# Performance work log

Hardware: AMD Instinct MI355X
Metric: run time of the kernel (lower is better)

## Reference

```python
import jax, jax.numpy as jnp
import numpy as np

N_VOCAB = 100      # periodic-table embedding size
N_GAUSS = 300      # SchNet-standard RBF expansion
RBF_CUTOFF = 30.0
RBF_GAMMA = 10.0
N_INTERACTIONS = 3
LOG2 = float(np.log(2.0))


def ssp(x):
    # shifted softplus: log(0.5*exp(x) + 0.5) = softplus(x) - log(2)
    return jax.nn.softplus(x) - LOG2


def setup_inputs() -> dict:
    key = jax.random.key(0)
    ks = jax.random.split(key, 16)
    B, N, F, NF = 32, 128, 128, 128
    s = lambda k, shape, sc=0.1: (jax.random.normal(k, shape, dtype=jnp.float32) * sc)
    return {
        "z": jax.random.randint(ks[0], (B, N), 0, N_VOCAB),
        "r": jax.random.normal(ks[1], (B, N, 3), dtype=jnp.float32) * 3.0,
        "emb": s(ks[2], (N_VOCAB, F)),
        "w_in2f": s(ks[3], (F, NF)),
        "w_f1": s(ks[4], (N_GAUSS, NF)), "b_f1": jnp.zeros((NF,), jnp.float32),
        "w_f2": s(ks[5], (NF, NF)),      "b_f2": jnp.zeros((NF,), jnp.float32),
        "w_f2out": s(ks[6], (NF, F)),    "b_f2out": jnp.zeros((F,), jnp.float32),
        "w_out": s(ks[7], (F, F)),       "b_out": jnp.zeros((F,), jnp.float32),
        "w_aw1": s(ks[8], (F, F)),       "b_aw1": jnp.zeros((F,), jnp.float32),
        "w_aw2": s(ks[9], (F, 1)),       "b_aw2": jnp.zeros((1,), jnp.float32),
    }


def reference(z, r, emb, w_in2f, w_f1, b_f1, w_f2, b_f2,
              w_f2out, b_f2out, w_out, b_out, w_aw1, b_aw1, w_aw2, b_aw2):
    # ---- pairwise distances + RBF expansion (shared across interactions) ----
    diff = r[:, :, None, :] - r[:, None, :, :]            # [B,N,N,3]
    d = jnp.sqrt(jnp.sum(diff * diff, axis=-1) + 1e-12)    # [B,N,N]
    centers = jnp.linspace(0.0, RBF_CUTOFF, N_GAUSS, dtype=jnp.float32)
    rbf = jnp.exp(-RBF_GAMMA * (d[..., None] - centers) ** 2)  # [B,N,N,G]
    # filter network (distance-only -> hoisted out of the interaction loop;
    # the single InteractionLayer is weight-shared across all passes)
    W = ssp(jnp.einsum('bijg,gf->bijf', rbf, w_f1) + b_f1)
    W = jnp.einsum('bijf,fh->bijh', W, w_f2) + b_f2         # [B,N,N,NF]

    # ---- atom embedding ----
    x = emb[z]                                              # [B,N,F]

    # ---- interaction blocks (shared weights, applied n_interactions times) ----
    for _ in range(N_INTERACTIONS):
        f = jnp.einsum('bnf,fh->bnh', x, w_in2f)            # atom-wise, no bias
        y = jnp.einsum('bijh,bjh->bih', W, f)               # cfconv aggregation
        y = ssp(jnp.einsum('bnh,hf->bnf', y, w_f2out) + b_f2out)
        v = jnp.einsum('bnf,fg->bng', y, w_out) + b_out
        x = x + v                                           # residual update

    # ---- atom-wise readout ----
    x = ssp(jnp.einsum('bnf,fg->bng', x, w_aw1) + b_aw1)
    out = jnp.einsum('bnf,fo->bno', x, w_aw2) + b_aw2       # [B,N,1]
    return out
```

## Files before the change

kernel.cpp:

```cpp
#include <hip/hip_runtime.h>
#include <hip/hip_bf16.h>
#include <stdint.h>

typedef __bf16 bf16x8 __attribute__((ext_vector_type(8)));
typedef float  f32x4  __attribute__((ext_vector_type(4)));
typedef unsigned short u16;
typedef unsigned int   u32;
typedef u16 u16x4 __attribute__((ext_vector_type(4)));
typedef u32 u32x4 __attribute__((ext_vector_type(4)));

#define B_  32
#define N_  128
#define F_  128
#define G_  300
#define GP  320
#define TAB_N 4096
#define TAB_SCALE 128.0f

__device__ __forceinline__ u16 f2b(float f){
  union { float f; u32 u; } x; x.f = f;
  u32 r = x.u + 0x7FFFu + ((x.u >> 16) & 1u);
  return (u16)(r >> 16);
}
__device__ __forceinline__ u32 pack2bf(float a, float b){
  return __builtin_amdgcn_perm(__float_as_uint(b) + 0x8000u,
                               __float_as_uint(a) + 0x8000u, 0x07060302u);
}
__device__ __forceinline__ float sspf(float x){
  return fmaxf(x, 0.0f) + __logf(0.5f + 0.5f*__expf(-fabsf(x)));
}
__device__ __forceinline__ f32x4 mfma16(bf16x8 a, bf16x8 b, f32x4 c){
  return __builtin_amdgcn_mfma_f32_16x16x32_bf16(a, b, c, 0, 0, 0);
}

__global__ __launch_bounds__(256) void k_setup(const float* __restrict__ w_f1,
                                               const float* __restrict__ w_f2,
                                               const float* __restrict__ w_in2f,
                                               const float* __restrict__ w_f2out,
                                               const float* __restrict__ w_out,
                                               const float* __restrict__ w_aw1,
                                               u16* __restrict__ w1t,
                                               u16* __restrict__ w2t,
                                               u16* __restrict__ wi2t,
                                               u16* __restrict__ w2outT,
                                               u16* __restrict__ woutT,
                                               u16* __restrict__ waw1T){
  int idx = blockIdx.x*256 + threadIdx.x;
  if (idx < 128*GP){
    int h = idx / GP, g = idx % GP;
    w1t[idx] = (g < G_) ? f2b(w_f1[g*F_ + h]) : (u16)0;
  } else {
    int j = idx - 128*GP;
    int which = j >> 14;
    int rr = j & 16383;
    int h = rr >> 7, k = rr & 127;
    const float* src; u16* dst;
    switch (which){
      case 0:  src = w_f2;    dst = w2t;    break;
      case 1:  src = w_in2f;  dst = wi2t;   break;
      case 2:  src = w_f2out; dst = w2outT; break;
      case 3:  src = w_out;   dst = woutT;  break;
      default: src = w_aw1;   dst = waw1T;  break;
    }
    dst[h*128 + k] = f2b(src[k*128 + h]);
  }
}

__global__ __launch_bounds__(256) void k_prep(const u16* __restrict__ w1t,
                                              const u16* __restrict__ w2t,
                                              const float* __restrict__ b_f1,
                                              const float* __restrict__ b_f2,
                                              u16* __restrict__ tab,
                                              const int* __restrict__ z,
                                              const float* __restrict__ emb,
                                              const u16* __restrict__ wi2t,
                                              u16* __restrict__ fb,
                                              const float* __restrict__ r,
                                              u16* __restrict__ dIdx){
  __shared__ __attribute__((aligned(16))) u16 w1s[16][136];
  __shared__ float rshp[128][3];
  int blk = blockIdx.x;
  int tid = threadIdx.x, lane = tid & 63, wave = tid >> 6;
  int m = lane & 15, q = lane >> 4;

  if (blk < 256){
    int t0 = blk * 16;
    int C0 = wave*32;
    const float K2 = 14.4269504089f;
    const float DC = 30.0f/299.0f;
    float d = (float)(t0 + m) * (1.0f/TAB_SCALE);
    f32x4 acc[2];
    acc[0] = (f32x4){0.f,0.f,0.f,0.f}; acc[1] = (f32x4){0.f,0.f,0.f,0.f};
    #pragma unroll
    for (int ks = 0; ks < 10; ++ks){
      int kb = ks*32 + q*8;
      u32x4 au;
      #pragma unroll
      for (int t2 = 0; t2 < 4; ++t2){
        int k0 = kb + t2*2;
        float u0 = d - DC*(float)k0;
        float u1 = d - DC*(float)(k0 + 1);
        float e0 = __builtin_amdgcn_exp2f(-K2*u0*u0);
        float e1 = __builtin_amdgcn_exp2f(-K2*u1*u1);
        au[t2] = pack2bf(e0, e1);
      }
      bf16x8 af = __builtin_bit_cast(bf16x8, au);
      #pragma unroll
      for (int ni = 0; ni < 2; ++ni){
        bf16x8 bfv = *reinterpret_cast<const bf16x8*>(w1t + (size_t)(C0 + ni*16 + m)*GP + kb);
        acc[ni] = mfma16(af, bfv, acc[ni]);
      }
    }
    #pragma unroll
    for (int ni = 0; ni < 2; ++ni)
      #pragma unroll
      for (int rr = 0; rr < 4; ++rr){
        int col = C0 + ni*16 + m;
        w1s[q*4 + rr][col & 127] = f2b(sspf(acc[ni][rr] + b_f1[col]));
      }
    __syncthreads();
    f32x4 acc2[2];
    acc2[0] = (f32x4){0.f,0.f,0.f,0.f}; acc2[1] = (f32x4){0.f,0.f,0.f,0.f};
    #pragma unroll
    for (int ks = 0; ks < 4; ++ks){
      int kb = ks*32 + q*8;
      bf16x8 af = *reinterpret_cast<const bf16x8*>(&w1s[m][kb]);
      #pragma unroll
      for (int ni = 0; ni < 2; ++ni){
        bf16x8 bfv = *reinterpret_cast<const bf16x8*>(w2t + (size_t)(C0 + ni*16 + m)*128 + kb);
        acc2[ni] = mfma16(af, bfv, acc2[ni]);
      }
    }
    #pragma unroll
    for (int ni = 0; ni < 2; ++ni)
      #pragma unroll
      for (int rr = 0; rr < 4; ++rr){
        int col = C0 + ni*16 + m;
        tab[(size_t)(t0 + q*4 + rr)*F_ + col] = f2b(acc2[ni][rr] + b_f2[col]);
      }
  } else if (blk < 384){
    int bi = blk - 256;
    int b = bi >> 2, qd = bi & 3;
    int R0 = qd*32 + (wave >> 1)*16;
    int C0 = (wave & 1)*64;
    int row = R0 + m;
    const float* erow = emb + (size_t)z[b*N_ + row]*F_;
    f32x4 acc[4];
    #pragma unroll
    for (int ni = 0; ni < 4; ++ni) acc[ni] = (f32x4){0.f,0.f,0.f,0.f};
    #pragma unroll
    for (int ks = 0; ks < 4; ++ks){
      int k0 = ks*32 + q*8;
      float4 e0 = *reinterpret_cast<const float4*>(erow + k0);
      float4 e1 = *reinterpret_cast<const float4*>(erow + k0 + 4);
      u32x4 au;
      au[0] = pack2bf(e0.x, e0.y); au[1] = pack2bf(e0.z, e0.w);
      au[2] = pack2bf(e1.x, e1.y); au[3] = pack2bf(e1.z, e1.w);
      bf16x8 af = __builtin_bit_cast(bf16x8, au);
      #pragma unroll
      for (int ni = 0; ni < 4; ++ni){
        bf16x8 bfv = *reinterpret_cast<const bf16x8*>(wi2t + (size_t)(C0 + ni*16 + m)*F_ + k0);
        acc[ni] = mfma16(af, bfv, acc[ni]);
      }
    }
    u16* fbb = fb + (size_t)b*N_*F_;
    #pragma unroll
    for (int ni = 0; ni < 4; ++ni)
      #pragma unroll
      for (int rr = 0; rr < 4; ++rr)
        fbb[(size_t)(R0 + q*4 + rr)*F_ + C0 + ni*16 + m] = f2b(acc[ni][rr]);
  } else {
    int pb = blk - 384;
    int b = pb >> 1, i0p = (pb & 1)*64;
    if (tid < 128){
      const float* rp = r + (size_t)(b*N_ + tid)*3;
      rshp[tid][0] = rp[0]; rshp[tid][1] = rp[1]; rshp[tid][2] = rp[2];
    }
    __syncthreads();
    #pragma unroll
    for (int t = 0; t < 32; ++t){
      int p = t*256 + tid;
      int il = p >> 7, j = p & 127;
      int i = i0p + il;
      float dx = rshp[i][0] - rshp[j][0];
      float dy = rshp[i][1] - rshp[j][1];
      float dz = rshp[i][2] - rshp[j][2];
      float d = sqrtf(fmaf(dx,dx, fmaf(dy,dy, fmaf(dz,dz, 1e-12f))));
      int ix = (int)(d * TAB_SCALE + 0.5f);
      if (ix > TAB_N - 1) ix = TAB_N - 1;
      dIdx[((size_t)(b*N_ + i))*N_ + j] = (u16)ix;
    }
  }
}

__global__ __launch_bounds__(256, 8) void k_conv(const u16* __restrict__ fb,
                                                 const u16* __restrict__ tab,
                                                 const u16* __restrict__ dIdx,
                                                 u16* __restrict__ yb){
  __shared__ u16 dIdxS[2][128];
  __shared__ __attribute__((aligned(16))) float psh[8][2][128];
  int bid = blockIdx.x;
  int b = bid >> 6, i0 = (bid & 63)*2;
  int tid = threadIdx.x;
  {
    int il = tid >> 7, j = tid & 127;
    dIdxS[il][j] = dIdx[((size_t)(b*N_ + i0 + il))*N_ + j];
  }
  __syncthreads();

  int chg = tid & 15, il = (tid >> 4) & 1, jq = tid >> 5;
  int h0 = chg*8;
  const u16* tb0 = tab + h0;
  const u16* fbp = fb + (size_t)b*N_*F_ + h0;
  float yv[8] = {0,0,0,0,0,0,0,0};
  #pragma unroll 8
  for (int jj = 0; jj < 16; ++jj){
    int j = jq*16 + jj;
    u32 ix = dIdxS[il][j];
    bf16x8 ta = *reinterpret_cast<const bf16x8*>(tb0 + ((size_t)ix << 7));
    bf16x8 fv = *reinterpret_cast<const bf16x8*>(fbp + (size_t)j*F_);
    #pragma unroll
    for (int t = 0; t < 8; ++t)
      yv[t] = fmaf((float)ta[t], (float)fv[t], yv[t]);
  }
  {
    float* pp = &psh[jq][il][h0];
    *reinterpret_cast<float4*>(pp)     = (float4){yv[0], yv[1], yv[2], yv[3]};
    *reinterpret_cast<float4*>(pp + 4) = (float4){yv[4], yv[5], yv[6], yv[7]};
  }
  __syncthreads();
  int ilo = tid >> 7, cho = tid & 127;
  float s = 0.f;
  #pragma unroll
  for (int t = 0; t < 8; ++t) s += psh[t][ilo][cho];
  yb[((size_t)(b*N_ + i0 + ilo))*F_ + cho] = f2b(s);
}

__global__ __launch_bounds__(512) void k_mlp(const u16* __restrict__ yb,
                                             float* __restrict__ x,
                                             const int* __restrict__ z,
                                             const float* __restrict__ emb,
                                             const u16* __restrict__ w2outT,
                                             const float* __restrict__ b_f2out,
                                             const u16* __restrict__ woutT,
                                             const float* __restrict__ b_out,
                                             const u16* __restrict__ wi2t,
                                             const u16* __restrict__ waw1T,
                                             const float* __restrict__ b_aw1,
                                             const float* __restrict__ w_aw2,
                                             const float* __restrict__ b_aw2,
                                             u16* __restrict__ fb,
                                             float* __restrict__ outp,
                                             int first, int mode){
  __shared__ __attribute__((aligned(16))) u16 ab[16][136];
  __shared__ float cs[16][132];
  __shared__ float psum[16][8];
  __shared__ int zsh[16];
  int tid = threadIdx.x, lane = tid & 63, wave = tid >> 6;
  int m = lane & 15, q = lane >> 4;
  int bid = blockIdx.x;
  int b = bid >> 3, R0 = (bid & 7)*16;
  int C0 = wave*16;
  int col = C0 + m;

  if (first && tid < 16) zsh[tid] = z[b*N_ + R0 + tid];
  {
    int row = tid >> 5, c4 = (tid & 31)*4;
    *reinterpret_cast<u16x4*>(&ab[row][c4]) =
      *reinterpret_cast<const u16x4*>(yb + ((size_t)(b*N_ + R0 + row))*F_ + c4);
  }
  __syncthreads();

  f32x4 acc = (f32x4){0.f,0.f,0.f,0.f};
  #pragma unroll
  for (int ks = 0; ks < 4; ++ks){
    int kb = ks*32 + q*8;
    bf16x8 af = *reinterpret_cast<const bf16x8*>(&ab[m][kb]);
    bf16x8 bfv = *reinterpret_cast<const bf16x8*>(w2outT + (size_t)col*F_ + kb);
    acc = mfma16(af, bfv, acc);
  }
  __syncthreads();
  #pragma unroll
  for (int rr = 0; rr < 4; ++rr)
    ab[q*4 + rr][col] = f2b(sspf(acc[rr] + b_f2out[col]));
  __syncthreads();

  f32x4 acc2 = (f32x4){0.f,0.f,0.f,0.f};
  #pragma unroll
  for (int ks = 0; ks < 4; ++ks){
    int kb = ks*32 + q*8;
    bf16x8 af = *reinterpret_cast<const bf16x8*>(&ab[m][kb]);
    bf16x8 bfv = *reinterpret_cast<const bf16x8*>(woutT + (size_t)col*F_ + kb);
    acc2 = mfma16(af, bfv, acc2);
  }
  __syncthreads();
  #pragma unroll
  for (int rr = 0; rr < 4; ++rr){
    int row = q*4 + rr;
    size_t xo = (size_t)(b*N_ + R0 + row)*F_ + col;
    float xi = first ? emb[(size_t)zsh[row]*F_ + col] : x[xo];
    float nv = xi + acc2[rr] + b_out[col];
    if (mode == 0) x[xo] = nv;
    ab[row][col] = f2b(nv);
  }
  __syncthreads();

  const u16* w3 = (mode == 0) ? wi2t : waw1T;
  f32x4 acc3 = (f32x4){0.f,0.f,0.f,0.f};
  #pragma unroll
  for (int ks = 0; ks < 4; ++ks){
    int kb = ks*32 + q*8;
    bf16x8 af = *reinterpret_cast<const bf16x8*>(&ab[m][kb]);
    bf16x8 bfv = *reinterpret_cast<const bf16x8*>(w3 + (size_t)col*F_ + kb);
    acc3 = mfma16(af, bfv, acc3);
  }
  if (mode == 0){
    #pragma unroll
    for (int rr = 0; rr < 4; ++rr)
      fb[(size_t)(b*N_ + R0 + q*4 + rr)*F_ + col] = f2b(acc3[rr]);
  } else {
    #pragma unroll
    for (int rr = 0; rr < 4; ++rr)
      cs[q*4 + rr][col] = sspf(acc3[rr] + b_aw1[col]) * w_aw2[col];
    __syncthreads();
    if (tid < 128){
      int row = tid >> 3, seg = tid & 7;
      float s = 0.f;
      #pragma unroll
      for (int t = 0; t < 16; ++t) s += cs[row][seg*16 + t];
      psum[row][seg] = s;
    }
    __syncthreads();
    if (tid < 16){
      float s = 0.f;
      #pragma unroll
      for (int t = 0; t < 8; ++t) s += psum[tid][t];
      outp[b*N_ + R0 + tid] = s + b_aw2[0];
    }
  }
}

extern "C" void kernel_launch(void* const* d_in, const int* in_sizes, int n_in,
                              void* d_out, int out_size, void* d_ws, size_t ws_size,
                              hipStream_t stream){
  const int*   z       = (const int*)d_in[0];
  const float* r       = (const float*)d_in[1];
  const float* emb     = (const float*)d_in[2];
  const float* w_in2f  = (const float*)d_in[3];
  const float* w_f1    = (const float*)d_in[4];
  const float* b_f1    = (const float*)d_in[5];
  const float* w_f2    = (const float*)d_in[6];
  const float* b_f2    = (const float*)d_in[7];
  const float* w_f2out = (const float*)d_in[8];
  const float* b_f2out = (const float*)d_in[9];
  const float* w_out   = (const float*)d_in[10];
  const float* b_out   = (const float*)d_in[11];
  const float* w_aw1   = (const float*)d_in[12];
  const float* b_aw1   = (const float*)d_in[13];
  const float* w_aw2   = (const float*)d_in[14];
  const float* b_aw2   = (const float*)d_in[15];

  char* ws = (char*)d_ws;
  float* x     = (float*)(ws);
  u16*   yb    = (u16*)(ws + 2097152);
  u16*   fbuf  = (u16*)(ws + 3145728);
  u16*   tab   = (u16*)(ws + 4194304);
  u16*   dIdx  = (u16*)(ws + 5242880);
  u16*   w1t   = (u16*)(ws + 6291456);
  u16*   w2t   = (u16*)(ws + 6373376);
  u16*   wi2t  = (u16*)(ws + 6406144);
  u16*   w2oT  = (u16*)(ws + 6438912);
  u16*   woT   = (u16*)(ws + 6471680);
  u16*   waw1T = (u16*)(ws + 6504448);

  k_setup<<<480, 256, 0, stream>>>(w_f1, w_f2, w_in2f, w_f2out, w_out, w_aw1,
                                   w1t, w2t, wi2t, w2oT, woT, waw1T);
  k_prep<<<448, 256, 0, stream>>>(w1t, w2t, b_f1, b_f2, tab,
                                  z, emb, wi2t, fbuf, r, dIdx);
  k_conv<<<2048, 256, 0, stream>>>(fbuf, tab, dIdx, yb);
  k_mlp<<<256, 512, 0, stream>>>(yb, x, z, emb, w2oT, b_f2out, woT, b_out,
                                 wi2t, waw1T, b_aw1, w_aw2, b_aw2,
                                 fbuf, (float*)d_out, 1, 0);
  k_conv<<<2048, 256, 0, stream>>>(fbuf, tab, dIdx, yb);
  k_mlp<<<256, 512, 0, stream>>>(yb, x, z, emb, w2oT, b_f2out, woT, b_out,
                                 wi2t, waw1T, b_aw1, w_aw2, b_aw2,
                                 fbuf, (float*)d_out, 0, 0);
  k_conv<<<2048, 256, 0, stream>>>(fbuf, tab, dIdx, yb);
  k_mlp<<<256, 512, 0, stream>>>(yb, x, z, emb, w2oT, b_f2out, woT, b_out,
                                 wi2t, waw1T, b_aw1, w_aw2, b_aw2,
                                 fbuf, (float*)d_out, 0, 1);
}
```

Before: 146.8 us.

## Fuse cfconv aggregation and atom-wise MLP into one per-iteration kernel

```diff
diff --git a/kernel.cpp b/kernel.cpp
--- a/kernel.cpp
+++ b/kernel.cpp
@@ -21,6 +21,9 @@
   union { float f; u32 u; } x; x.f = f;
   u32 r = x.u + 0x7FFFu + ((x.u >> 16) & 1u);
   return (u16)(r >> 16);
+}
+__device__ __forceinline__ float b2f(u16 v){
+  union { u32 u; float f; } x; x.u = ((u32)v) << 16; return x.f;
 }
 __device__ __forceinline__ u32 pack2bf(float a, float b){
   return __builtin_amdgcn_perm(__float_as_uint(b) + 0x8000u,
@@ -42,27 +45,31 @@
                                                u16* __restrict__ w1t,
                                                u16* __restrict__ w2t,
                                                u16* __restrict__ wi2t,
-                                               u16* __restrict__ w2outT,
-                                               u16* __restrict__ woutT,
-                                               u16* __restrict__ waw1T){
+                                               u16* __restrict__ wf2o,
+                                               u16* __restrict__ wob,
+                                               u16* __restrict__ wi2fb,
+                                               u16* __restrict__ waw1b){
   int idx = blockIdx.x*256 + threadIdx.x;
   if (idx < 128*GP){
     int h = idx / GP, g = idx % GP;
     w1t[idx] = (g < G_) ? f2b(w_f1[g*F_ + h]) : (u16)0;
+  } else if (idx < 128*GP + 32768){
+    int j = idx - 128*GP;
+    int which = j >> 14, rr = j & 16383;
+    int h = rr >> 7, k = rr & 127;
+    if (which == 0) w2t[h*128 + k]  = f2b(w_f2[k*128 + h]);
+    else            wi2t[h*128 + k] = f2b(w_in2f[k*128 + h]);
   } else {
-    int j = idx - 128*GP;
-    int which = j >> 14;
-    int rr = j & 16383;
-    int h = rr >> 7, k = rr & 127;
+    int j = idx - 128*GP - 32768;
+    int which = j >> 14, rr = j & 16383;
     const float* src; u16* dst;
     switch (which){
-      case 0:  src = w_f2;    dst = w2t;    break;
-      case 1:  src = w_in2f;  dst = wi2t;   break;
-      case 2:  src = w_f2out; dst = w2outT; break;
-      case 3:  src = w_out;   dst = woutT;  break;
-      default: src = w_aw1;   dst = waw1T;  break;
-    }
-    dst[h*128 + k] = f2b(src[k*128 + h]);
+      case 0:  src = w_f2out; dst = wf2o;  break;
+      case 1:  src = w_out;   dst = wob;   break;
+      case 2:  src = w_in2f;  dst = wi2fb; break;
+      default: src = w_aw1;   dst = waw1b; break;
+    }
+    dst[rr] = f2b(src[rr]);
   }
 }
 
@@ -193,12 +200,22 @@
   }
 }
 
-__global__ __launch_bounds__(256, 8) void k_conv(const u16* __restrict__ fb,
-                                                 const u16* __restrict__ tab,
-                                                 const u16* __restrict__ dIdx,
-                                                 u16* __restrict__ yb){
+__global__ __launch_bounds__(256, 8) void k_iter(
+    const u16* __restrict__ fb_in, const u16* __restrict__ tab,
+    const u16* __restrict__ dIdx,
+    float* __restrict__ x, const int* __restrict__ z,
+    const float* __restrict__ emb,
+    const u16* __restrict__ wf2o, const float* __restrict__ b_f2out,
+    const u16* __restrict__ wob,  const float* __restrict__ b_out,
+    const u16* __restrict__ wi2fb, const u16* __restrict__ waw1b,
+    const float* __restrict__ b_aw1, const float* __restrict__ w_aw2,
+    const float* __restrict__ b_aw2,
+    u16* __restrict__ fb_out, float* __restrict__ outp, int first, int mode){
   __shared__ u16 dIdxS[2][128];
   __shared__ __attribute__((aligned(16))) float psh[8][2][128];
+  __shared__ float ysh[2][132];
+  __shared__ float y2sh[2][132];
+  __shared__ float xsh[2][132];
   int bid = blockIdx.x;
   int b = bid >> 6, i0 = (bid & 63)*2;
   int tid = threadIdx.x;
@@ -208,134 +225,114 @@
   }
   __syncthreads();
 
-  int chg = tid & 15, il = (tid >> 4) & 1, jq = tid >> 5;
-  int h0 = chg*8;
-  const u16* tb0 = tab + h0;
-  const u16* fbp = fb + (size_t)b*N_*F_ + h0;
-  float yv[8] = {0,0,0,0,0,0,0,0};
-  #pragma unroll 8
-  for (int jj = 0; jj < 16; ++jj){
-    int j = jq*16 + jj;
-    u32 ix = dIdxS[il][j];
-    bf16x8 ta = *reinterpret_cast<const bf16x8*>(tb0 + ((size_t)ix << 7));
-    bf16x8 fv = *reinterpret_cast<const bf16x8*>(fbp + (size_t)j*F_);
-    #pragma unroll
-    for (int t = 0; t < 8; ++t)
-      yv[t] = fmaf((float)ta[t], (float)fv[t], yv[t]);
-  }
-  {
+  {
+    int chg = tid & 15, il = (tid >> 4) & 1, jq = tid >> 5;
+    int h0 = chg*8;
+    const u16* tb0 = tab + h0;
+    const u16* fbp = fb_in + (size_t)b*N_*F_ + h0;
+    float yv[8] = {0,0,0,0,0,0,0,0};
+    #pragma unroll 8
+    for (int jj = 0; jj < 16; ++jj){
+      int j = jq*16 + jj;
+      u32 ix = dIdxS[il][j];
+      bf16x8 ta = *reinterpret_cast<const bf16x8*>(tb0 + ((size_t)ix << 7));
+      bf16x8 fv = *reinterpret_cast<const bf16x8*>(fbp + (size_t)j*F_);
+      #pragma unroll
+      for (int t = 0; t < 8; ++t)
+        yv[t] = fmaf((float)ta[t], (float)fv[t], yv[t]);
+    }
     float* pp = &psh[jq][il][h0];
     *reinterpret_cast<float4*>(pp)     = (float4){yv[0], yv[1], yv[2], yv[3]};
     *reinterpret_cast<float4*>(pp + 4) = (float4){yv[4], yv[5], yv[6], yv[7]};
   }
   __syncthreads();
-  int ilo = tid >> 7, cho = tid & 127;
-  float s = 0.f;
-  #pragma unroll
-  for (int t = 0; t < 8; ++t) s += psh[t][ilo][cho];
-  yb[((size_t)(b*N_ + i0 + ilo))*F_ + cho] = f2b(s);
-}
-
-__global__ __launch_bounds__(512) void k_mlp(const u16* __restrict__ yb,
-                                             float* __restrict__ x,
-                                             const int* __restrict__ z,
-                                             const float* __restrict__ emb,
-                                             const u16* __restrict__ w2outT,
-                                             const float* __restrict__ b_f2out,
-                                             const u16* __restrict__ woutT,
-                                             const float* __restrict__ b_out,
-                                             const u16* __restrict__ wi2t,
-                                             const u16* __restrict__ waw1T,
-                                             const float* __restrict__ b_aw1,
-                                             const float* __restrict__ w_aw2,
-                                             const float* __restrict__ b_aw2,
-                                             u16* __restrict__ fb,
-                                             float* __restrict__ outp,
-                                             int first, int mode){
-  __shared__ __attribute__((aligned(16))) u16 ab[16][136];
-  __shared__ float cs[16][132];
-  __shared__ float psum[16][8];
-  __shared__ int zsh[16];
-  int tid = threadIdx.x, lane = tid & 63, wave = tid >> 6;
-  int m = lane & 15, q = lane >> 4;
-  int bid = blockIdx.x;
-  int b = bid >> 3, R0 = (bid & 7)*16;
-  int C0 = wave*16;
-  int col = C0 + m;
-
-  if (first && tid < 16) zsh[tid] = z[b*N_ + R0 + tid];
-  {
-    int row = tid >> 5, c4 = (tid & 31)*4;
-    *reinterpret_cast<u16x4*>(&ab[row][c4]) =
-      *reinterpret_cast<const u16x4*>(yb + ((size_t)(b*N_ + R0 + row))*F_ + c4);
-  }
-  __syncthreads();
-
-  f32x4 acc = (f32x4){0.f,0.f,0.f,0.f};
-  #pragma unroll
-  for (int ks = 0; ks < 4; ++ks){
-    int kb = ks*32 + q*8;
-    bf16x8 af = *reinterpret_cast<const bf16x8*>(&ab[m][kb]);
-    bf16x8 bfv = *reinterpret_cast<const bf16x8*>(w2outT + (size_t)col*F_ + kb);
-    acc = mfma16(af, bfv, acc);
-  }
-  __syncthreads();
-  #pragma unroll
-  for (int rr = 0; rr < 4; ++rr)
-    ab[q*4 + rr][col] = f2b(sspf(acc[rr] + b_f2out[col]));
-  __syncthreads();
-
-  f32x4 acc2 = (f32x4){0.f,0.f,0.f,0.f};
-  #pragma unroll
-  for (int ks = 0; ks < 4; ++ks){
-    int kb = ks*32 + q*8;
-    bf16x8 af = *reinterpret_cast<const bf16x8*>(&ab[m][kb]);
-    bf16x8 bfv = *reinterpret_cast<const bf16x8*>(woutT + (size_t)col*F_ + kb);
-    acc2 = mfma16(af, bfv, acc2);
-  }
-  __syncthreads();
-  #pragma unroll
-  for (int rr = 0; rr < 4; ++rr){
-    int row = q*4 + rr;
-    size_t xo = (size_t)(b*N_ + R0 + row)*F_ + col;
-    float xi = first ? emb[(size_t)zsh[row]*F_ + col] : x[xo];
-    float nv = xi + acc2[rr] + b_out[col];
+  {
+    int ilo = tid >> 7, cho = tid & 127;
+    float s = 0.f;
+    #pragma unroll
+    for (int t = 0; t < 8; ++t) s += psh[t][ilo][cho];
+    ysh[ilo][cho] = s;
+  }
+  __syncthreads();
+
+  int kh = tid >> 7, col = tid & 127;
+  int k0 = kh*64;
+  float* psum = &psh[0][0][0];
+
+  {
+    float a0 = 0.f, a1 = 0.f;
+    #pragma unroll 8
+    for (int kk = 0; kk < 64; ++kk){
+      int k = k0 + kk;
+      float w = b2f(wf2o[k*F_ + col]);
+      a0 = fmaf(ysh[0][k], w, a0);
+      a1 = fmaf(ysh[1][k], w, a1);
+    }
+    psum[(kh*2    )*128 + col] = a0;
+    psum[(kh*2 + 1)*128 + col] = a1;
+  }
+  __syncthreads();
+  { int row = tid >> 7, c = tid & 127;
+    y2sh[row][c] = sspf(psum[row*128 + c] + psum[(2 + row)*128 + c] + b_f2out[c]); }
+  __syncthreads();
+
+  {
+    float a0 = 0.f, a1 = 0.f;
+    #pragma unroll 8
+    for (int kk = 0; kk < 64; ++kk){
+      int k = k0 + kk;
+      float w = b2f(wob[k*F_ + col]);
+      a0 = fmaf(y2sh[0][k], w, a0);
+      a1 = fmaf(y2sh[1][k], w, a1);
+    }
+    psum[(kh*2    )*128 + col] = a0;
+    psum[(kh*2 + 1)*128 + col] = a1;
+  }
+  __syncthreads();
+  { int row = tid >> 7, c = tid & 127;
+    size_t xo = (size_t)(b*N_ + i0 + row)*F_ + c;
+    float xi = first ? emb[(size_t)z[b*N_ + i0 + row]*F_ + c] : x[xo];
+    float nv = xi + psum[row*128 + c] + psum[(2 + row)*128 + c] + b_out[c];
     if (mode == 0) x[xo] = nv;
-    ab[row][col] = f2b(nv);
-  }
-  __syncthreads();
-
-  const u16* w3 = (mode == 0) ? wi2t : waw1T;
-  f32x4 acc3 = (f32x4){0.f,0.f,0.f,0.f};
-  #pragma unroll
-  for (int ks = 0; ks < 4; ++ks){
-    int kb = ks*32 + q*8;
-    bf16x8 af = *reinterpret_cast<const bf16x8*>(&ab[m][kb]);
-    bf16x8 bfv = *reinterpret_cast<const bf16x8*>(w3 + (size_t)col*F_ + kb);
-    acc3 = mfma16(af, bfv, acc3);
-  }
+    xsh[row][c] = nv; }
+  __syncthreads();
+
+  const u16* w3 = (mode == 0) ? wi2fb : waw1b;
+  {
+    float a0 = 0.f, a1 = 0.f;
+    #pragma unroll 8
+    for (int kk = 0; kk < 64; ++kk){
+      int k = k0 + kk;
+      float w = b2f(w3[k*F_ + col]);
+      a0 = fmaf(xsh[0][k], w, a0);
+      a1 = fmaf(xsh[1][k], w, a1);
+    }
+    psum[(kh*2    )*128 + col] = a0;
+    psum[(kh*2 + 1)*128 + col] = a1;
+  }
+  __syncthreads();
   if (mode == 0){
-    #pragma unroll
-    for (int rr = 0; rr < 4; ++rr)
-      fb[(size_t)(b*N_ + R0 + q*4 + rr)*F_ + col] = f2b(acc3[rr]);
+    int row = tid >> 7, c = tid & 127;
+    fb_out[(size_t)(b*N_ + i0 + row)*F_ + c] =
+      f2b(psum[row*128 + c] + psum[(2 + row)*128 + c]);
   } else {
-    #pragma unroll
-    for (int rr = 0; rr < 4; ++rr)
-      cs[q*4 + rr][col] = sspf(acc3[rr] + b_aw1[col]) * w_aw2[col];
+    { int row = tid >> 7, c = tid & 127;
+      y2sh[row][c] = sspf(psum[row*128 + c] + psum[(2 + row)*128 + c] + b_aw1[c])
+                     * w_aw2[c]; }
     __syncthreads();
-    if (tid < 128){
-      int row = tid >> 3, seg = tid & 7;
+    if (tid < 64){
+      int row = tid >> 5, seg = tid & 31;
       float s = 0.f;
       #pragma unroll
-      for (int t = 0; t < 16; ++t) s += cs[row][seg*16 + t];
-      psum[row][seg] = s;
+      for (int t = 0; t < 4; ++t) s += y2sh[row][seg*4 + t];
+      psum[row*32 + seg] = s;
     }
     __syncthreads();
-    if (tid < 16){
+    if (tid < 2){
       float s = 0.f;
       #pragma unroll
-      for (int t = 0; t < 8; ++t) s += psum[tid][t];
-      outp[b*N_ + R0 + tid] = s + b_aw2[0];
+      for (int t = 0; t < 32; ++t) s += psum[tid*32 + t];
+      outp[b*N_ + i0 + tid] = s + b_aw2[0];
     }
   }
 }
@@ -362,31 +359,32 @@
 
   char* ws = (char*)d_ws;
   float* x     = (float*)(ws);
-  u16*   yb    = (u16*)(ws + 2097152);
-  u16*   fbuf  = (u16*)(ws + 3145728);
+  u16*   f0    = (u16*)(ws + 2097152);
+  u16*   f1    = (u16*)(ws + 3145728);
   u16*   tab   = (u16*)(ws + 4194304);
   u16*   dIdx  = (u16*)(ws + 5242880);
   u16*   w1t   = (u16*)(ws + 6291456);
   u16*   w2t   = (u16*)(ws + 6373376);
   u16*   wi2t  = (u16*)(ws + 6406144);
-  u16*   w2oT  = (u16*)(ws + 6438912);
-  u16*   woT   = (u16*)(ws + 6471680);
-  u16*   waw1T = (u16*)(ws + 6504448);
-
-  k_setup<<<480, 256, 0, stream>>>(w_f1, w_f2, w_in2f, w_f2out, w_out, w_aw1,
-                                   w1t, w2t, wi2t, w2oT, woT, waw1T);
+  u16*   wf2o  = (u16*)(ws + 6438912);
+  u16*   wob   = (u16*)(ws + 6471680);
+  u16*   wi2fb = (u16*)(ws + 6504448);
+  u16*   waw1b = (u16*)(ws + 6537216);
+
+  k_setup<<<544, 256, 0, stream>>>(w_f1, w_f2, w_in2f, w_f2out, w_out, w_aw1,
+                                   w1t, w2t, wi2t, wf2o, wob, wi2fb, waw1b);
   k_prep<<<448, 256, 0, stream>>>(w1t, w2t, b_f1, b_f2, tab,
-                                  z, emb, wi2t, fbuf, r, dIdx);
-  k_conv<<<2048, 256, 0, stream>>>(fbuf, tab, dIdx, yb);
-  k_mlp<<<256, 512, 0, stream>>>(yb, x, z, emb, w2oT, b_f2out, woT, b_out,
-                                 wi2t, waw1T, b_aw1, w_aw2, b_aw2,
-                                 fbuf, (float*)d_out, 1, 0);
-  k_conv<<<2048, 256, 0, stream>>>(fbuf, tab, dIdx, yb);
-  k_mlp<<<256, 512, 0, stream>>>(yb, x, z, emb, w2oT, b_f2out, woT, b_out,
-                                 wi2t, waw1T, b_aw1, w_aw2, b_aw2,
-                                 fbuf, (float*)d_out, 0, 0);
-  k_conv<<<2048, 256, 0, stream>>>(fbuf, tab, dIdx, yb);
-  k_mlp<<<256, 512, 0, stream>>>(yb, x, z, emb, w2oT, b_f2out, woT, b_out,
-                                 wi2t, waw1T, b_aw1, w_aw2, b_aw2,
-                                 fbuf, (float*)d_out, 0, 1);
-}
+                                  z, emb, wi2t, f0, r, dIdx);
+  k_iter<<<2048, 256, 0, stream>>>(f0, tab, dIdx, x, z, emb,
+                                   wf2o, b_f2out, wob, b_out, wi2fb, waw1b,
+                                   b_aw1, w_aw2, b_aw2,
+                                   f1, (float*)d_out, 1, 0);
+  k_iter<<<2048, 256, 0, stream>>>(f1, tab, dIdx, x, z, emb,
+                                   wf2o, b_f2out, wob, b_out, wi2fb, waw1b,
+                                   b_aw1, w_aw2, b_aw2,
+                                   f0, (float*)d_out, 0, 0);
+  k_iter<<<2048, 256, 0, stream>>>(f0, tab, dIdx, x, z, emb,
+                                   wf2o, b_f2out, wob, b_out, wi2fb, waw1b,
+                                   b_aw1, w_aw2, b_aw2,
+                                   f1, (float*)d_out, 0, 1);
+}
```

New measurement: 205.6 us. 1.4x slower.
